# Performance work log

Measured on AMD Instinct MI355X. Metric: run time of the kernel, lower is better.

The kernel has to match this reference:

```python
import jax, jax.numpy as jnp
import numpy as np

HS = 2048   # hidden_size
NH = 16     # num_attention_heads
HD = HS // NH  # head_dim = 128
FD = 256    # feature_dim
EPS = 1e-5  # layer_norm_epsilon


def setup_inputs() -> dict:
    key = jax.random.key(0)
    ks = jax.random.split(key, 12)
    s = 0.02
    return {
        "hidden_states": jax.random.normal(ks[0], (2, 4096, HS), jnp.float32),
        "attention_mask": jnp.zeros((2, 4096), jnp.float32),
        "Wq": jax.random.normal(ks[1], (HS, HS), jnp.float32) * s,
        "bq": jnp.zeros((HS,), jnp.float32),
        "Wk": jax.random.normal(ks[2], (HS, HS), jnp.float32) * s,
        "bk": jnp.zeros((HS,), jnp.float32),
        "Wv": jax.random.normal(ks[3], (HS, HS), jnp.float32) * s,
        "bv": jnp.zeros((HS,), jnp.float32),
        "Wo": jax.random.normal(ks[4], (HS, HS), jnp.float32) * s,
        "bo": jnp.zeros((HS,), jnp.float32),
        "Wf1": jax.random.normal(ks[5], (HD, FD), jnp.float32) * s,
        "bf1": jnp.zeros((FD,), jnp.float32),
        "Wf2": jax.random.normal(ks[6], (FD, FD), jnp.float32) * s,
        "bf2": jnp.zeros((FD,), jnp.float32),
        "ln_g": jnp.ones((FD,), jnp.float32),
        "ln_b": jnp.zeros((FD,), jnp.float32),
    }


def reference(hidden_states, attention_mask, Wq, bq, Wk, bk, Wv, bv, Wo, bo,
              Wf1, bf1, Wf2, bf2, ln_g, ln_b):
    B, L, H = hidden_states.shape

    # QKV projections -> [B, NH, L, HD]
    q = (hidden_states @ Wq + bq).reshape(B, L, NH, HD).transpose(0, 2, 1, 3)
    k = (hidden_states @ Wk + bk).reshape(B, L, NH, HD).transpose(0, 2, 1, 3)
    v = (hidden_states @ Wv + bv).reshape(B, L, NH, HD).transpose(0, 2, 1, 3)

    # seq_len (4096) > linear_threshold (1024) -> linear attention branch
    def feature_map(x):  # Linear -> ReLU -> Linear -> LayerNorm
        h = jax.nn.relu(x @ Wf1 + bf1)
        h = h @ Wf2 + bf2
        mu = jnp.mean(h, axis=-1, keepdims=True)
        var = jnp.var(h, axis=-1, keepdims=True)  # biased, like torch LayerNorm
        return (h - mu) * jax.lax.rsqrt(var + EPS) * ln_g + ln_b

    q_feat = feature_map(q)  # [B, NH, L, FD]
    k_feat = feature_map(k)
    # attention_mask [B, L] -> k_feat * (1 + mask)
    k_feat = k_feat * (1.0 + attention_mask[:, None, :, None])

    kv = jnp.einsum('bhlf,bhld->bhfd', k_feat, v)          # [B, NH, FD, HD]
    attn = jnp.einsum('bhlf,bhfd->bhld', q_feat, kv)       # [B, NH, L, HD]
    k_sum = jnp.sum(k_feat, axis=2)                         # [B, NH, FD]
    denom = jnp.einsum('bhlf,bhf->bhl', q_feat, k_sum)[..., None]
    attn = attn / (denom + 1e-8)

    attn = attn.transpose(0, 2, 1, 3).reshape(B, L, H)
    return attn @ Wo + bo
```

## Files before the change

kernel.cpp:

```cpp
#include <hip/hip_runtime.h>

typedef unsigned short u16;
typedef unsigned int u32;
typedef __attribute__((ext_vector_type(8))) short bf16x8;
typedef __attribute__((ext_vector_type(4))) float f32x4;

#define B_ 2
#define L_ 4096
#define HS_ 2048
#define NH_ 16
#define HD_ 128
#define FD_ 256

__device__ __forceinline__ float bf2f(u16 u) { return __uint_as_float(((u32)u) << 16); }
__device__ __forceinline__ u16 f2bf(float f) {
    u32 x = __float_as_uint(f);
    return (u16)((x + 0x7fffu + ((x >> 16) & 1u)) >> 16);
}

__device__ __forceinline__ void llds16(const u16* g, u16* l) {
    __builtin_amdgcn_global_load_lds((const __attribute__((address_space(1))) void*)g,
                                     (__attribute__((address_space(3))) void*)l, 16, 0, 0);
}

__device__ __forceinline__ void gemm_mainloop(const u16* __restrict__ Ab, int lda,
                                              const u16* __restrict__ Bb, int ldb,
                                              int K, u16* As, u16* Bs, f32x4 (&acc)[4][4]) {
    const int tid  = threadIdx.x;
    const int lane = tid & 63;
    const int wave = tid >> 6;
    const int wm = wave >> 1, wn = wave & 1;

    f32x4 zero = {0.f, 0.f, 0.f, 0.f};
#pragma unroll
    for (int i = 0; i < 4; i++)
#pragma unroll
        for (int j = 0; j < 4; j++) acc[i][j] = zero;

    const int srow = lane >> 2;
    const int scol = (lane & 3) * 8;
    const u16* pa = Ab + (size_t)(wave * 32 + srow) * lda + scol;
    const u16* pb = Bb + (size_t)(wave * 32 + srow) * ldb + scol;
    u16* la = As + wave * 1024;
    u16* lb = Bs + wave * 1024;

    const int arow = (wm * 64 + (lane & 15)) * 32 + (lane >> 4) * 8;
    const int brow = (wn * 64 + (lane & 15)) * 32 + (lane >> 4) * 8;

    for (int k0 = 0; k0 < K; k0 += 32) {
        llds16(pa, la);
        llds16(pa + 16 * lda, la + 512);
        llds16(pb, lb);
        llds16(pb + 16 * ldb, lb + 512);
        pa += 32; pb += 32;
        __syncthreads();
        bf16x8 af[4], bg[4];
#pragma unroll
        for (int mt = 0; mt < 4; mt++) af[mt] = *(const bf16x8*)(As + arow + mt * 512);
#pragma unroll
        for (int nt = 0; nt < 4; nt++) bg[nt] = *(const bf16x8*)(Bs + brow + nt * 512);
#pragma unroll
        for (int mt = 0; mt < 4; mt++)
#pragma unroll
            for (int nt = 0; nt < 4; nt++)
                acc[mt][nt] = __builtin_amdgcn_mfma_f32_16x16x32_bf16(af[mt], bg[nt], acc[mt][nt], 0, 0, 0);
        __syncthreads();
    }
}

__global__ __launch_bounds__(256) void k_cvt(const float* __restrict__ src, u16* __restrict__ dst) {
    size_t i = ((size_t)blockIdx.x * 256 + threadIdx.x) * 8;
    float4 a = *(const float4*)(src + i);
    float4 b = *(const float4*)(src + i + 4);
    union { u16 h[8]; uint4 v; } o;
    o.h[0] = f2bf(a.x); o.h[1] = f2bf(a.y); o.h[2] = f2bf(a.z); o.h[3] = f2bf(a.w);
    o.h[4] = f2bf(b.x); o.h[5] = f2bf(b.y); o.h[6] = f2bf(b.z); o.h[7] = f2bf(b.w);
    *(uint4*)(dst + i) = o.v;
}

__global__ __launch_bounds__(256) void k_transpose(const float* Wq, const float* Wk, const float* Wv,
                                                   const float* Wo, const float* Wf1, const float* Wf2,
                                                   u16* Wqkv_t, u16* Wo_t, u16* Wf1_t, u16* Wf2_t) {
    const float* src; u16* dst; int R, C;
    switch (blockIdx.z) {
        case 0: src = Wq;  dst = Wqkv_t;                R = 2048; C = 2048; break;
        case 1: src = Wk;  dst = Wqkv_t + 2048 * 2048;  R = 2048; C = 2048; break;
        case 2: src = Wv;  dst = Wqkv_t + 2 * 2048 * 2048; R = 2048; C = 2048; break;
        case 3: src = Wo;  dst = Wo_t;                  R = 2048; C = 2048; break;
        case 4: src = Wf1; dst = Wf1_t;                 R = 128;  C = 256;  break;
        default: src = Wf2; dst = Wf2_t;                R = 256;  C = 256;  break;
    }
    int c0 = blockIdx.x * 32, r0 = blockIdx.y * 32;
    if (c0 >= C || r0 >= R) return;
    __shared__ u16 tile[32][33];
    int tx = threadIdx.x, ty = threadIdx.y;
    for (int i = ty; i < 32; i += 8) tile[i][tx] = f2bf(src[(size_t)(r0 + i) * C + c0 + tx]);
    __syncthreads();
    for (int i = ty; i < 32; i += 8) dst[(size_t)(c0 + i) * R + r0 + tx] = tile[tx][i];
}

__global__ __launch_bounds__(256) void k_gemm_qkv(const u16* __restrict__ X, const u16* __restrict__ Wt,
                                                  const float* __restrict__ bq, const float* __restrict__ bk,
                                                  const float* __restrict__ bv,
                                                  u16* __restrict__ qb, u16* __restrict__ kb, u16* __restrict__ vT) {
    __shared__ u16 S[128 * 132];
    f32x4 acc[4][4];
    const int bid = blockIdx.y * 64 + blockIdx.x;
    const int mblk = (bid / 384) * 8 + (bid & 7);
    const int nblk = (bid >> 3) % 48;
    const int mb = mblk * 128, nb = nblk * 128;
    gemm_mainloop(X + (size_t)mb * HS_, HS_, Wt + (size_t)nb * HS_, HS_, HS_, S, S + 4096, acc);
    const int tid = threadIdx.x, lane = tid & 63, wave = tid >> 6;
    const int wm = wave >> 1, wn = wave & 1;
    const int which = nb >> 11;
    const int col0 = nb & 2047;
    const int h = col0 >> 7;
    const int b = mb >> 12;
    const int lb = mb & 4095;
    const int bh = b * NH_ + h;
    const float* bias = (which == 0) ? bq : (which == 1 ? bk : bv);
    const int mloc = wm * 64 + ((lane >> 4) << 2);
    const int nloc = wn * 64 + (lane & 15);
    if (which < 2) {
#pragma unroll
        for (int nt = 0; nt < 4; nt++) {
            float bvv = bias[col0 + nloc + nt * 16];
#pragma unroll
            for (int mt = 0; mt < 4; mt++)
#pragma unroll
                for (int r = 0; r < 4; r++)
                    S[(mloc + mt * 16 + r) * 132 + nloc + nt * 16] = f2bf(acc[mt][nt][r] + bvv);
        }
    } else {
#pragma unroll
        for (int nt = 0; nt < 4; nt++) {
            float bvv = bias[col0 + nloc + nt * 16];
#pragma unroll
            for (int mt = 0; mt < 4; mt++)
#pragma unroll
                for (int r = 0; r < 4; r++)
                    S[(nloc + nt * 16) * 132 + mloc + mt * 16 + r] = f2bf(acc[mt][nt][r] + bvv);
        }
    }
    __syncthreads();
    u16* dst = (which == 0) ? qb : (which == 1 ? kb : vT);
    const int c8 = (tid & 15) * 8;
#pragma unroll
    for (int it = 0; it < 8; it++) {
        int row = (tid >> 4) + it * 16;
        uint2 lo = *(const uint2*)(S + row * 132 + c8);
        uint2 hi = *(const uint2*)(S + row * 132 + c8 + 4);
        uint4 val = make_uint4(lo.x, lo.y, hi.x, hi.y);
        u16* p = (which < 2) ? dst + ((size_t)bh * L_ + lb + row) * HD_ + c8
                             : dst + ((size_t)bh * HD_ + row) * L_ + lb + c8;
        *(uint4*)p = val;
    }
}

template <int MASKED, int TRANS>
__global__ __launch_bounds__(256) void k_feat(const u16* __restrict__ X,
                                              const u16* __restrict__ W1t, const float* __restrict__ b1,
                                              const u16* __restrict__ W2t, const float* __restrict__ b2,
                                              const float* __restrict__ g, const float* __restrict__ be,
                                              const float* __restrict__ mask,
                                              u16* __restrict__ feat, float* __restrict__ ksp) {
    __shared__ u16 As[64 * 32];
    __shared__ u16 Bs[256 * 32];
    __shared__ u16 H[64 * 264];
    __shared__ float MU[64], RS[64], FAC[64];
    const int tid = threadIdx.x, lane = tid & 63, wave = tid >> 6;
    const int mb = blockIdx.x * 64;

    const int srow = lane >> 2, scol = (lane & 3) * 8;
    const int arow_rd = (lane & 15);
    const int kgrp = (lane >> 4) * 8;

    f32x4 acc[4][4];
    f32x4 zero = {0.f, 0.f, 0.f, 0.f};
#pragma unroll
    for (int i = 0; i < 4; i++)
#pragma unroll
        for (int j = 0; j < 4; j++) acc[i][j] = zero;

    for (int k0 = 0; k0 < 128; k0 += 32) {
        llds16(X + (size_t)(mb + wave * 16 + srow) * 128 + k0 + scol, As + wave * 512);
#pragma unroll
        for (int i = 0; i < 4; i++)
            llds16(W1t + (size_t)((wave * 4 + i) * 16 + srow) * 128 + k0 + scol,
                   Bs + (wave * 4 + i) * 512);
        __syncthreads();
        bf16x8 af[4], bg[4];
#pragma unroll
        for (int mt = 0; mt < 4; mt++) af[mt] = *(const bf16x8*)(As + (mt * 16 + arow_rd) * 32 + kgrp);
#pragma unroll
        for (int nt = 0; nt < 4; nt++) bg[nt] = *(const bf16x8*)(Bs + (wave * 64 + nt * 16 + arow_rd) * 32 + kgrp);
#pragma unroll
        for (int mt = 0; mt < 4; mt++)
#pragma unroll
            for (int nt = 0; nt < 4; nt++)
                acc[mt][nt] = __builtin_amdgcn_mfma_f32_16x16x32_bf16(af[mt], bg[nt], acc[mt][nt], 0, 0, 0);
        __syncthreads();
    }
    {
        const int rbase = (lane >> 4) << 2;
#pragma unroll
        for (int nt = 0; nt < 4; nt++) {
            int n = wave * 64 + nt * 16 + (lane & 15);
            float bvv = b1[n];
#pragma unroll
            for (int mt = 0; mt < 4; mt++)
#pragma unroll
                for (int r = 0; r < 4; r++) {
                    float v = fmaxf(acc[mt][nt][r] + bvv, 0.f);
                    H[(mt * 16 + rbase + r) * 264 + n] = f2bf(v);
                }
            acc[0][nt] = zero; acc[1][nt] = zero; acc[2][nt] = zero; acc[3][nt] = zero;
        }
    }
    __syncthreads();

    for (int k0 = 0; k0 < 256; k0 += 32) {
#pragma unroll
        for (int i = 0; i < 4; i++)
            llds16(W2t + (size_t)((wave * 4 + i) * 16 + srow) * 256 + k0 + scol,
                   Bs + (wave * 4 + i) * 512);
        __syncthreads();
        bf16x8 af[4], bg[4];
#pragma unroll
        for (int mt = 0; mt < 4; mt++) af[mt] = *(const bf16x8*)(H + (mt * 16 + arow_rd) * 264 + k0 + kgrp);
#pragma unroll
        for (int nt = 0; nt < 4; nt++) bg[nt] = *(const bf16x8*)(Bs + (wave * 64 + nt * 16 + arow_rd) * 32 + kgrp);
#pragma unroll
        for (int mt = 0; mt < 4; mt++)
#pragma unroll
            for (int nt = 0; nt < 4; nt++)
                acc[mt][nt] = __builtin_amdgcn_mfma_f32_16x16x32_bf16(af[mt], bg[nt], acc[mt][nt], 0, 0, 0);
        __syncthreads();
    }
    {
        const int rbase = (lane >> 4) << 2;
#pragma unroll
        for (int nt = 0; nt < 4; nt++) {
            int n = wave * 64 + nt * 16 + (lane & 15);
            float bvv = b2[n];
#pragma unroll
            for (int mt = 0; mt < 4; mt++)
#pragma unroll
                for (int r = 0; r < 4; r++)
                    H[(mt * 16 + rbase + r) * 264 + n] = f2bf(acc[mt][nt][r] + bvv);
        }
    }
    __syncthreads();

    {
        for (int r = 0; r < 16; r++) {
            int row = wave * 16 + r;
            int j = lane * 4;
            uint2 u = *(const uint2*)(H + row * 264 + j);
            float x0 = bf2f((u16)(u.x & 0xffff)), x1 = bf2f((u16)(u.x >> 16));
            float x2 = bf2f((u16)(u.y & 0xffff)), x3 = bf2f((u16)(u.y >> 16));
            float s = x0 + x1 + x2 + x3;
            float ss = x0 * x0 + x1 * x1 + x2 * x2 + x3 * x3;
#pragma unroll
            for (int o = 32; o >= 1; o >>= 1) { s += __shfl_xor(s, o); ss += __shfl_xor(ss, o); }
            if (lane == 0) {
                float mu = s * (1.f / FD_);
                float var = ss * (1.f / FD_) - mu * mu;
                MU[row] = mu;
                RS[row] = rsqrtf(var + 1e-5f);
                float fac = 1.f;
                if (MASKED) {
                    int grow = mb + row;
                    int b = grow >> 16;
                    int l = grow & 4095;
                    fac = 1.f + mask[b * L_ + l];
                }
                FAC[row] = fac;
            }
        }
    }
    __syncthreads();

    if (!TRANS) {
        int j = lane * 4;
        float4 gg = *(const float4*)(g + j);
        float4 bb = *(const float4*)(be + j);
        for (int r = 0; r < 16; r++) {
            int row = wave * 16 + r;
            float mu = MU[row], rstd = RS[row], fac = FAC[row];
            uint2 u = *(const uint2*)(H + row * 264 + j);
            float x0 = bf2f((u16)(u.x & 0xffff)), x1 = bf2f((u16)(u.x >> 16));
            float x2 = bf2f((u16)(u.y & 0xffff)), x3 = bf2f((u16)(u.y >> 16));
            uint2 o2;
            o2.x = (u32)f2bf(((x0 - mu) * rstd * gg.x + bb.x) * fac) |
                   ((u32)f2bf(((x1 - mu) * rstd * gg.y + bb.y) * fac) << 16);
            o2.y = (u32)f2bf(((x2 - mu) * rstd * gg.z + bb.z) * fac) |
                   ((u32)f2bf(((x3 - mu) * rstd * gg.w + bb.w) * fac) << 16);
            *(uint2*)(feat + (size_t)(mb + row) * FD_ + j) = o2;
        }
    } else {
        int f = tid;
        int bh = mb >> 12, lb = mb & 4095;
        float gf = g[f], bf = be[f];
        u16* orow = feat + ((size_t)bh * FD_ + f) * L_ + lb;
        float fsum = 0.f;
        for (int lg = 0; lg < 64; lg += 8) {
            union { u16 h8[8]; uint4 v4; } pk;
#pragma unroll
            for (int j = 0; j < 8; j++) {
                int row = lg + j;
                float x = bf2f(H[row * 264 + f]);
                float y = ((x - MU[row]) * RS[row] * gf + bf) * FAC[row];
                fsum += y;
                pk.h8[j] = f2bf(y);
            }
            *(uint4*)(orow + lg) = pk.v4;
        }
        ksp[((size_t)bh * 64 + (lb >> 6)) * FD_ + f] = fsum;
    }
}

__global__ __launch_bounds__(256) void k_ksum2(const float* __restrict__ ksp, float* __restrict__ ksum) {
    const int bh = blockIdx.x, f = threadIdx.x;
    float s = 0.f;
    for (int i = 0; i < 64; i++) s += ksp[((size_t)bh * 64 + i) * FD_ + f];
    ksum[(size_t)bh * FD_ + f] = s;
}

__global__ __launch_bounds__(256) void k_gemm_kv(const u16* __restrict__ kfT, const u16* __restrict__ vT,
                                                 float* __restrict__ kvp) {
    __shared__ u16 As[4096], Bs[4096];
    f32x4 acc[4][4];
    const int mb = blockIdx.x * 128;
    const int ks = blockIdx.y;
    const int bh = blockIdx.z;
    gemm_mainloop(kfT + ((size_t)bh * FD_ + mb) * L_ + ks * 512, L_,
                  vT + (size_t)bh * HD_ * L_ + ks * 512, L_, 512, As, Bs, acc);
    const int lane = threadIdx.x & 63, wave = threadIdx.x >> 6;
    const int wm = wave >> 1, wn = wave & 1;
    const int n0 = wn * 64 + (lane & 15);
    const int m0 = mb + wm * 64 + ((lane >> 4) << 2);
    float* o = kvp + (size_t)(ks * 32 + bh) * (FD_ * HD_);
#pragma unroll
    for (int nt = 0; nt < 4; nt++)
#pragma unroll
        for (int mt = 0; mt < 4; mt++)
#pragma unroll
            for (int r = 0; r < 4; r++)
                o[(size_t)(m0 + mt * 16 + r) * HD_ + n0 + nt * 16] = acc[mt][nt][r];
}

__global__ __launch_bounds__(256) void k_kvred(const float* __restrict__ kvp, u16* __restrict__ kvT) {
    const int p = blockIdx.x, bh = blockIdx.y, t = threadIdx.x;
    const int e0 = p * 4096 + t * 16;
    float s[16];
#pragma unroll
    for (int i = 0; i < 16; i++) s[i] = 0.f;
    for (int c = 0; c < 8; c++) {
        const float* src = kvp + ((size_t)(c * 32 + bh)) * 32768 + e0;
#pragma unroll
        for (int i = 0; i < 16; i += 4) {
            float4 vv = *(const float4*)(src + i);
            s[i] += vv.x; s[i + 1] += vv.y; s[i + 2] += vv.z; s[i + 3] += vv.w;
        }
    }
#pragma unroll
    for (int i = 0; i < 16; i++) {
        int e = e0 + i, fq = e >> 7, d = e & 127;
        kvT[((size_t)bh * HD_ + d) * FD_ + fq] = f2bf(s[i]);
    }
}

__global__ __launch_bounds__(256) void k_denom(const u16* __restrict__ qf, const float* __restrict__ ksum,
                                               float* __restrict__ denom) {
    const int lane = threadIdx.x & 63, wave = threadIdx.x >> 6;
    const size_t row = (size_t)blockIdx.x * 4 + wave;
    const int bh = (int)(row >> 12);
    uint2 u = *(const uint2*)(qf + row * FD_ + lane * 4);
    float4 kk = *(const float4*)(ksum + (size_t)bh * FD_ + lane * 4);
    float d = bf2f((u16)(u.x & 0xffff)) * kk.x + bf2f((u16)(u.x >> 16)) * kk.y
            + bf2f((u16)(u.y & 0xffff)) * kk.z + bf2f((u16)(u.y >> 16)) * kk.w;
#pragma unroll
    for (int o = 32; o >= 1; o >>= 1) d += __shfl_xor(d, o);
    if (lane == 0) denom[row] = d;
}

__global__ __launch_bounds__(256) void k_gemm_attn(const u16* __restrict__ qf, const u16* __restrict__ kvT,
                                                   const float* __restrict__ denom, u16* __restrict__ attn) {
    __shared__ u16 S[128 * 132];
    f32x4 acc[4][4];
    const int mb = blockIdx.x * 128;
    const int bh = blockIdx.y;
    gemm_mainloop(qf + ((size_t)bh * L_ + mb) * FD_, FD_, kvT + (size_t)bh * HD_ * FD_, FD_, FD_, S, S + 4096, acc);
    const int tid = threadIdx.x, lane = tid & 63, wave = tid >> 6;
    const int wm = wave >> 1, wn = wave & 1;
    const int b = bh >> 4, h = bh & 15;
    const int mloc = wm * 64 + ((lane >> 4) << 2);
    const int nloc = wn * 64 + (lane & 15);
#pragma unroll
    for (int mt = 0; mt < 4; mt++)
#pragma unroll
        for (int r = 0; r < 4; r++) {
            int l = mb + mloc + mt * 16 + r;
            float rden = 1.f / (denom[(size_t)bh * L_ + l] + 1e-8f);
#pragma unroll
            for (int nt = 0; nt < 4; nt++)
                S[(mloc + mt * 16 + r) * 132 + nloc + nt * 16] = f2bf(acc[mt][nt][r] * rden);
        }
    __syncthreads();
    const int c8 = (tid & 15) * 8;
#pragma unroll
    for (int it = 0; it < 8; it++) {
        int row = (tid >> 4) + it * 16;
        uint2 lo = *(const uint2*)(S + row * 132 + c8);
        uint2 hi = *(const uint2*)(S + row * 132 + c8 + 4);
        uint4 val = make_uint4(lo.x, lo.y, hi.x, hi.y);
        *(uint4*)(attn + ((size_t)(b * L_ + mb + row)) * HS_ + h * HD_ + c8) = val;
    }
}

__global__ __launch_bounds__(256) void k_gemm_out(const u16* __restrict__ A, const u16* __restrict__ Wt,
                                                  const float* __restrict__ bo, float* __restrict__ out) {
    __shared__ u16 As[4096], Bs[4096];
    f32x4 acc[4][4];
    const int bid = blockIdx.y * 64 + blockIdx.x;
    const int mblk = (bid / 128) * 8 + (bid & 7);
    const int nblk = (bid >> 3) % 16;
    const int mb = mblk * 128, nb = nblk * 128;
    gemm_mainloop(A + (size_t)mb * HS_, HS_, Wt + (size_t)nb * HS_, HS_, HS_, As, Bs, acc);
    const int lane = threadIdx.x & 63, wave = threadIdx.x >> 6;
    const int wm = wave >> 1, wn = wave & 1;
    const int n0 = nb + wn * 64 + (lane & 15);
    const int m0 = mb + wm * 64 + ((lane >> 4) << 2);
#pragma unroll
    for (int nt = 0; nt < 4; nt++) {
        int n = n0 + nt * 16;
        float bvv = bo[n];
#pragma unroll
        for (int mt = 0; mt < 4; mt++)
#pragma unroll
            for (int r = 0; r < 4; r++)
                out[(size_t)(m0 + mt * 16 + r) * HS_ + n] = acc[mt][nt][r] + bvv;
    }
}

extern "C" void kernel_launch(void* const* d_in, const int* in_sizes, int n_in,
                              void* d_out, int out_size, void* d_ws, size_t ws_size,
                              hipStream_t stream) {
    const float* hs  = (const float*)d_in[0];
    const float* msk = (const float*)d_in[1];
    const float* Wq  = (const float*)d_in[2];  const float* bq  = (const float*)d_in[3];
    const float* Wk  = (const float*)d_in[4];  const float* bk  = (const float*)d_in[5];
    const float* Wv  = (const float*)d_in[6];  const float* bv  = (const float*)d_in[7];
    const float* Wo  = (const float*)d_in[8];  const float* bo  = (const float*)d_in[9];
    const float* Wf1 = (const float*)d_in[10]; const float* bf1 = (const float*)d_in[11];
    const float* Wf2 = (const float*)d_in[12]; const float* bf2 = (const float*)d_in[13];
    const float* lng = (const float*)d_in[14]; const float* lnb = (const float*)d_in[15];
    float* out = (float*)d_out;
    char* w = (char*)d_ws;

    u16* qfeat  = (u16*)(w + 0);
    u16* Wqkv_t = (u16*)(w + 0);
    u16* Xbf    = (u16*)(w + 25165824u);
    u16* kfT    = (u16*)(w + 67108864u);
    u16* qbuf   = (u16*)(w + 134217728u);
    float* kvp  = (float*)(w + 134217728u);
    u16* kbuf   = (u16*)(w + 167772160u);
    u16* attn   = (u16*)(w + 167772160u);
    u16* vT     = (u16*)(w + 201326592u);
    u16* Wo_t   = (u16*)(w + 234881024u);
    u16* Wf1_t  = (u16*)(w + 243269632u);
    u16* Wf2_t  = (u16*)(w + 243335168u);
    float* ksp  = (float*)(w + 243466240u);
    u16* kvT    = (u16*)(w + 245563392u);
    float* ksum = (float*)(w + 247660544u);
    float* denom = (float*)(w + 247693312u);

    k_cvt<<<dim3(8192), 256, 0, stream>>>(hs, Xbf);
    k_transpose<<<dim3(64, 64, 6), dim3(32, 8), 0, stream>>>(Wq, Wk, Wv, Wo, Wf1, Wf2,
                                                             Wqkv_t, Wo_t, Wf1_t, Wf2_t);
    k_gemm_qkv<<<dim3(64, 48), 256, 0, stream>>>(Xbf, Wqkv_t, bq, bk, bv, qbuf, kbuf, vT);
    k_feat<0, 0><<<dim3(2048), 256, 0, stream>>>(qbuf, Wf1_t, bf1, Wf2_t, bf2, lng, lnb, msk, qfeat, ksp);
    k_feat<1, 1><<<dim3(2048), 256, 0, stream>>>(kbuf, Wf1_t, bf1, Wf2_t, bf2, lng, lnb, msk, kfT, ksp);
    k_ksum2<<<dim3(32), 256, 0, stream>>>(ksp, ksum);
    k_gemm_kv<<<dim3(2, 8, 32), 256, 0, stream>>>(kfT, vT, kvp);
    k_kvred<<<dim3(8, 32), 256, 0, stream>>>(kvp, kvT);
    k_denom<<<dim3(32768), 256, 0, stream>>>(qfeat, ksum, denom);
    k_gemm_attn<<<dim3(32, 32), 256, 0, stream>>>(qfeat, kvT, denom, attn);
    k_gemm_out<<<dim3(64, 16), 256, 0, stream>>>(attn, Wo_t, bo, out);
}
```

Measured before the change: 809.2 us.

## Rewrite QKV GEMM with 256x256 tiles, 8 waves, and interleaved LDS prefetch

The QKV projection GEMM now uses 256x256 output tiles computed by 512 threads (8 waves), where it previously used 128x128 tiles with 256 threads. It double-buffers K-chunks of 64 in a 128KB LDS area with swizzled direct global-to-LDS loads. Prefetches are interleaved between MFMA phases with explicit barriers, sched_barriers and setprio. Block IDs are remapped per XCD for L2 locality, and the epilogue writes the tile in two halves through LDS. The goal is higher arithmetic intensity and better overlap of memory with matrix cores on the largest GEMM, at the cost of heavy register use (128 accumulator floats) and fragile manual scheduling.

Result: faster. 717.0 us (-11.4%).

```diff
diff --git a/kernel.cpp b/kernel.cpp
--- a/kernel.cpp
+++ b/kernel.cpp
@@ -99,61 +99,199 @@
     for (int i = ty; i < 32; i += 8) dst[(size_t)(c0 + i) * R + r0 + tx] = tile[tx][i];
 }
 
-__global__ __launch_bounds__(256) void k_gemm_qkv(const u16* __restrict__ X, const u16* __restrict__ Wt,
-                                                  const float* __restrict__ bq, const float* __restrict__ bk,
-                                                  const float* __restrict__ bv,
-                                                  u16* __restrict__ qb, u16* __restrict__ kb, u16* __restrict__ vT) {
-    __shared__ u16 S[128 * 132];
-    f32x4 acc[4][4];
-    const int bid = blockIdx.y * 64 + blockIdx.x;
-    const int mblk = (bid / 384) * 8 + (bid & 7);
-    const int nblk = (bid >> 3) % 48;
-    const int mb = mblk * 128, nb = nblk * 128;
-    gemm_mainloop(X + (size_t)mb * HS_, HS_, Wt + (size_t)nb * HS_, HS_, HS_, S, S + 4096, acc);
+#define QKV_BAR() { __builtin_amdgcn_sched_barrier(0); __builtin_amdgcn_s_barrier(); \
+                    __builtin_amdgcn_sched_barrier(0); }
+#define QKV_LGKM0() { asm volatile("s_waitcnt lgkmcnt(0)" ::: "memory"); \
+                      __builtin_amdgcn_sched_barrier(0); }
+
+__global__ __launch_bounds__(512, 2) void k_gemm_qkv(
+        const u16* __restrict__ X, const u16* __restrict__ Wt,
+        const float* __restrict__ bq, const float* __restrict__ bk, const float* __restrict__ bv,
+        u16* __restrict__ qout, u16* __restrict__ kout, u16* __restrict__ vT) {
+    __shared__ u16 LDS[65536];
     const int tid = threadIdx.x, lane = tid & 63, wave = tid >> 6;
-    const int wm = wave >> 1, wn = wave & 1;
-    const int which = nb >> 11;
-    const int col0 = nb & 2047;
-    const int h = col0 >> 7;
-    const int b = mb >> 12;
-    const int lb = mb & 4095;
-    const int bh = b * NH_ + h;
+    const int wm = wave >> 2, wn = wave & 3;
+
+    const int xcd = blockIdx.x & 7, idx = blockIdx.x >> 3;
+    const int nblk = idx >> 2;
+    const int mblk = xcd * 4 + (idx & 3);
+    const int mb = mblk * 256, nb = nblk * 256;
+
+    int r0g, c0g, r1g, c1g;
+    { int p = tid * 16; int s = p >> 10, q = p & 1023; q ^= ((q >> 9) & 1) << 5;
+      r0g = (s >> 1) * 16 + (q >> 6); c0g = (s & 1) * 32 + ((q & 63) >> 1); }
+    { int p = 8192 + tid * 16; int s = p >> 10, q = p & 1023; q ^= ((q >> 9) & 1) << 5;
+      r1g = (s >> 1) * 16 + (q >> 6); c1g = (s & 1) * 32 + ((q & 63) >> 1); }
+    const int voff0 = r0g * HS_ + c0g;
+    const int voff1 = r1g * HS_ + c1g;
+
+    int qby = (lane & 15) * 64 + (lane >> 4) * 16;
+    qby ^= ((qby >> 9) & 1) << 5;
+    const int qh = qby >> 1;
+
+#define STG(G, soff, dstu) { \
+    llds16((G) + (soff) + voff0, LDS + (dstu) + wave * 512); \
+    llds16((G) + (soff) + voff1, LDS + (dstu) + 4096 + wave * 512); }
+
+    const size_t a0 = (size_t)mb * HS_, a1 = (size_t)(mb + 128) * HS_;
+    const size_t b0 = (size_t)nb * HS_, b1 = (size_t)(nb + 128) * HS_;
+
+    STG(Wt, b0, 32768); STG(Wt, b1, 40960);
+    STG(X,  a0, 0);     STG(X,  a1, 8192);
+    STG(Wt, b0 + 64, 49152); STG(Wt, b1 + 64, 57344);
+    STG(X,  a0 + 64, 16384);
+    asm volatile("s_waitcnt vmcnt(6)" ::: "memory");
+    QKV_BAR();
+
+    f32x4 acc[8][4];
+    f32x4 zero = {0.f, 0.f, 0.f, 0.f};
+#pragma unroll
+    for (int i = 0; i < 8; i++)
+#pragma unroll
+        for (int j = 0; j < 4; j++) acc[i][j] = zero;
+
+    const int NT = HS_ / 64;
+    bf16x8 afr[4][2], bfr[4][2];
+    for (int t = 0; t < NT; t++) {
+        const int bsel = t & 1;
+        const u16* Ah = LDS + bsel * 16384 + wm * 8192;
+        const u16* Bh = LDS + 32768 + bsel * 16384 + (wn >> 1) * 8192;
+        const int bg0 = (wn & 1) * 4;
+        const size_t kc1 = (size_t)(t + 1) * 64, kc2 = (size_t)(t + 2) * 64;
+
+#pragma unroll
+        for (int mf = 0; mf < 4; mf++)
+#pragma unroll
+            for (int ks = 0; ks < 2; ks++)
+                afr[mf][ks] = *(const bf16x8*)(Ah + (mf * 2 + ks) * 512 + qh);
+#pragma unroll
+        for (int nf = 0; nf < 4; nf++)
+#pragma unroll
+            for (int ks = 0; ks < 2; ks++)
+                bfr[nf][ks] = *(const bf16x8*)(Bh + ((bg0 + nf) * 2 + ks) * 512 + qh);
+        if (t + 1 < NT) STG(X, a1 + kc1, (bsel ^ 1) * 16384 + 8192);
+        QKV_BAR();
+        QKV_LGKM0();
+        __builtin_amdgcn_s_setprio(1);
+#pragma unroll
+        for (int mf = 0; mf < 4; mf++)
+#pragma unroll
+            for (int nf = 0; nf < 2; nf++)
+#pragma unroll
+                for (int ks = 0; ks < 2; ks++)
+                    acc[mf][nf] = __builtin_amdgcn_mfma_f32_16x16x32_bf16(afr[mf][ks], bfr[nf][ks], acc[mf][nf], 0, 0, 0);
+        __builtin_amdgcn_s_setprio(0);
+        QKV_BAR();
+        if (t + 2 < NT) STG(Wt, b0 + kc2, 32768 + bsel * 16384);
+        QKV_BAR();
+        __builtin_amdgcn_s_setprio(1);
+#pragma unroll
+        for (int mf = 0; mf < 4; mf++)
+#pragma unroll
+            for (int nf = 2; nf < 4; nf++)
+#pragma unroll
+                for (int ks = 0; ks < 2; ks++)
+                    acc[mf][nf] = __builtin_amdgcn_mfma_f32_16x16x32_bf16(afr[mf][ks], bfr[nf][ks], acc[mf][nf], 0, 0, 0);
+        __builtin_amdgcn_s_setprio(0);
+        QKV_BAR();
+#pragma unroll
+        for (int mf = 0; mf < 4; mf++)
+#pragma unroll
+            for (int ks = 0; ks < 2; ks++)
+                afr[mf][ks] = *(const bf16x8*)(Ah + ((mf + 4) * 2 + ks) * 512 + qh);
+        if (t + 2 < NT) STG(Wt, b1 + kc2, 32768 + bsel * 16384 + 8192);
+        QKV_BAR();
+        QKV_LGKM0();
+        __builtin_amdgcn_s_setprio(1);
+#pragma unroll
+        for (int mf = 0; mf < 4; mf++)
+#pragma unroll
+            for (int nf = 0; nf < 2; nf++)
+#pragma unroll
+                for (int ks = 0; ks < 2; ks++)
+                    acc[mf + 4][nf] = __builtin_amdgcn_mfma_f32_16x16x32_bf16(afr[mf][ks], bfr[nf][ks], acc[mf + 4][nf], 0, 0, 0);
+        __builtin_amdgcn_s_setprio(0);
+        QKV_BAR();
+        if (t + 2 < NT) STG(X, a0 + kc2, bsel * 16384);
+        QKV_BAR();
+        __builtin_amdgcn_s_setprio(1);
+#pragma unroll
+        for (int mf = 0; mf < 4; mf++)
+#pragma unroll
+            for (int nf = 2; nf < 4; nf++)
+#pragma unroll
+                for (int ks = 0; ks < 2; ks++)
+                    acc[mf + 4][nf] = __builtin_amdgcn_mfma_f32_16x16x32_bf16(afr[mf][ks], bfr[nf][ks], acc[mf + 4][nf], 0, 0, 0);
+        __builtin_amdgcn_s_setprio(0);
+        if (t + 2 < NT) { asm volatile("s_waitcnt vmcnt(6)" ::: "memory"); }
+        else if (t + 1 < NT) { asm volatile("s_waitcnt vmcnt(0)" ::: "memory"); }
+        QKV_BAR();
+    }
+#undef STG
+
+    const int which = nblk >> 3;
+    const int colbase = (nblk & 7) * 256;
+    const int bi = mb >> 12, lb = mb & 4095;
     const float* bias = (which == 0) ? bq : (which == 1 ? bk : bv);
-    const int mloc = wm * 64 + ((lane >> 4) << 2);
-    const int nloc = wn * 64 + (lane & 15);
+    const int rb = (lane >> 4) << 2, cl = lane & 15;
+
     if (which < 2) {
-#pragma unroll
-        for (int nt = 0; nt < 4; nt++) {
-            float bvv = bias[col0 + nloc + nt * 16];
-#pragma unroll
-            for (int mt = 0; mt < 4; mt++)
-#pragma unroll
-                for (int r = 0; r < 4; r++)
-                    S[(mloc + mt * 16 + r) * 132 + nloc + nt * 16] = f2bf(acc[mt][nt][r] + bvv);
+        u16* dst = (which == 0) ? qout : kout;
+        const int bh0 = bi * NH_ + (colbase >> 7);
+        for (int half = 0; half < 2; half++) {
+            if (wm == half) {
+#pragma unroll
+                for (int nf = 0; nf < 4; nf++) {
+                    float bvv = bias[colbase + wn * 64 + nf * 16 + cl];
+#pragma unroll
+                    for (int mf = 0; mf < 8; mf++)
+#pragma unroll
+                        for (int r = 0; r < 4; r++)
+                            LDS[(mf * 16 + rb + r) * 264 + wn * 64 + nf * 16 + cl] =
+                                f2bf(acc[mf][nf][r] + bvv);
+                }
+            }
+            __syncthreads();
+#pragma unroll
+            for (int it = 0; it < 8; it++) {
+                int row = (tid >> 5) + it * 16;
+                int c8 = (tid & 31) * 8;
+                uint2 lo = *(const uint2*)(LDS + row * 264 + c8);
+                uint2 hi = *(const uint2*)(LDS + row * 264 + c8 + 4);
+                uint4 val = make_uint4(lo.x, lo.y, hi.x, hi.y);
+                u16* pp = dst + ((size_t)(bh0 + (c8 >> 7)) * L_ + lb + half * 128 + row) * HD_ + (c8 & 127);
+                *(uint4*)pp = val;
+            }
+            __syncthreads();
         }
     } else {
-#pragma unroll
-        for (int nt = 0; nt < 4; nt++) {
-            float bvv = bias[col0 + nloc + nt * 16];
-#pragma unroll
-            for (int mt = 0; mt < 4; mt++)
-#pragma unroll
-                for (int r = 0; r < 4; r++)
-                    S[(nloc + nt * 16) * 132 + mloc + mt * 16 + r] = f2bf(acc[mt][nt][r] + bvv);
-        }
-    }
-    __syncthreads();
-    u16* dst = (which == 0) ? qb : (which == 1 ? kb : vT);
-    const int c8 = (tid & 15) * 8;
-#pragma unroll
-    for (int it = 0; it < 8; it++) {
-        int row = (tid >> 4) + it * 16;
-        uint2 lo = *(const uint2*)(S + row * 132 + c8);
-        uint2 hi = *(const uint2*)(S + row * 132 + c8 + 4);
-        uint4 val = make_uint4(lo.x, lo.y, hi.x, hi.y);
-        u16* p = (which < 2) ? dst + ((size_t)bh * L_ + lb + row) * HD_ + c8
-                             : dst + ((size_t)bh * HD_ + row) * L_ + lb + c8;
-        *(uint4*)p = val;
+        for (int half = 0; half < 2; half++) {
+            if (wm == half) {
+#pragma unroll
+                for (int nf = 0; nf < 4; nf++) {
+                    float bvv = bias[colbase + wn * 64 + nf * 16 + cl];
+#pragma unroll
+                    for (int mf = 0; mf < 8; mf++)
+#pragma unroll
+                        for (int r = 0; r < 4; r++)
+                            LDS[(wn * 64 + nf * 16 + cl) * 136 + mf * 16 + rb + r] =
+                                f2bf(acc[mf][nf][r] + bvv);
+                }
+            }
+            __syncthreads();
+#pragma unroll
+            for (int it = 0; it < 8; it++) {
+                int n = (tid >> 4) + it * 32;
+                int c8 = (tid & 15) * 8;
+                uint2 lo = *(const uint2*)(LDS + n * 136 + c8);
+                uint2 hi = *(const uint2*)(LDS + n * 136 + c8 + 4);
+                uint4 val = make_uint4(lo.x, lo.y, hi.x, hi.y);
+                int cg = colbase + n;
+                u16* pp = vT + ((size_t)(bi * NH_ + (cg >> 7)) * HD_ + (cg & 127)) * L_ + lb + half * 128 + c8;
+                *(uint4*)pp = val;
+            }
+            __syncthreads();
+        }
     }
 }
 
@@ -479,7 +617,7 @@
     k_cvt<<<dim3(8192), 256, 0, stream>>>(hs, Xbf);
     k_transpose<<<dim3(64, 64, 6), dim3(32, 8), 0, stream>>>(Wq, Wk, Wv, Wo, Wf1, Wf2,
                                                              Wqkv_t, Wo_t, Wf1_t, Wf2_t);
-    k_gemm_qkv<<<dim3(64, 48), 256, 0, stream>>>(Xbf, Wqkv_t, bq, bk, bv, qbuf, kbuf, vT);
+    k_gemm_qkv<<<dim3(768), 512, 0, stream>>>(Xbf, Wqkv_t, bq, bk, bv, qbuf, kbuf, vT);
     k_feat<0, 0><<<dim3(2048), 256, 0, stream>>>(qbuf, Wf1_t, bf1, Wf2_t, bf2, lng, lnb, msk, qfeat, ksp);
     k_feat<1, 1><<<dim3(2048), 256, 0, stream>>>(kbuf, Wf1_t, bf1, Wf2_t, bf2, lng, lnb, msk, kfT, ksp);
     k_ksum2<<<dim3(32), 256, 0, stream>>>(ksp, ksum);
```
